# Performance work log

Measured on AMD Instinct MI355X. Metric: run time of the kernel, lower is better.

Reference implementation:

```python
import jax, jax.numpy as jnp
from jax import lax
import numpy as np

NODE_COUNT = 4096
BATCH = 128
THRESHOLD = 1.0
DISSIPATION = 0.1
SPARSITY = 0.9
MAX_ITERS = 100


def setup_inputs() -> dict:
    key = jax.random.key(0)
    k_in, k_conn, k_mask, k_w, k_b = jax.random.split(key, 5)
    input_data = jax.random.normal(k_in, (BATCH, NODE_COUNT), dtype=jnp.float32)
    conn = jax.random.normal(k_conn, (NODE_COUNT, NODE_COUNT), dtype=jnp.float32)
    mask = (jax.random.uniform(k_mask, (NODE_COUNT, NODE_COUNT)) > SPARSITY).astype(jnp.float32)
    conn = conn * mask
    conn = conn / (jnp.abs(conn).sum(axis=1, keepdims=True) + 1e-6)
    # input_proj: Linear(node_count, node_count), torch default init scale
    bound = 1.0 / np.sqrt(NODE_COUNT)
    W = jax.random.uniform(k_w, (NODE_COUNT, NODE_COUNT), minval=-bound, maxval=bound, dtype=jnp.float32)
    b = jax.random.uniform(k_b, (NODE_COUNT,), minval=-bound, maxval=bound, dtype=jnp.float32)
    return {"input_data": input_data, "W": W, "b": b, "connections": conn}


def _avalanche(state, connections):
    """Batched avalanche scan with per-sample sticky early-exit (torch break)."""
    B = state.shape[0]
    done0 = jnp.zeros((B,), dtype=bool)
    total0 = jnp.zeros((B,), dtype=state.dtype)

    def step(carry, _):
        state, done, total = carry
        active = (state > THRESHOLD).astype(state.dtype)          # [B, N]
        n_active = active.sum(axis=1)                              # [B]
        new_done = done | (n_active == 0)                          # break condition
        total = total + jnp.where(new_done, 0.0, n_active)
        # propagated = connections @ active  (per sample)
        prop = jnp.einsum('ij,bj->bi', connections, active)        # [B, N]
        new_state = (state * (1.0 - DISSIPATION) + prop * (1.0 - active)) * (1.0 - active)
        state = jnp.where(new_done[:, None], state, new_state)
        return (state, new_done, total), None

    (state, done, total), _ = lax.scan(step, (state, done0, total0), None, length=MAX_ITERS)
    return state, total


def reference(input_data, W, b, connections):
    projected = input_data @ W.T + b                               # [B, N]
    output, sizes = _avalanche(projected, connections)
    max_size = sizes.max()
    return output, max_size
```

## Files before the change

### kernel.cpp

```cpp
#include <hip/hip_runtime.h>

#define N_NODES 4096
#define BATCH 128
#define SPLITK 16
#define GBN 64
#define GBK 32
#define KCHUNK (N_NODES / SPLITK)
#define NSTEP (KCHUNK / GBK)
#define GEMM_BLOCKS ((N_NODES / GBN) * SPLITK)
#define TRANS_BLOCKS (32 * 32)

typedef _Float16 f16x4 __attribute__((ext_vector_type(4)));
typedef _Float16 f16x8 __attribute__((ext_vector_type(8)));
typedef float f32x4 __attribute__((ext_vector_type(4)));
typedef unsigned int u32x4 __attribute__((ext_vector_type(4)));

__device__ __forceinline__ void dma16(const void* g, void* l) {
#if defined(__has_builtin) && __has_builtin(__builtin_amdgcn_global_load_lds)
  __builtin_amdgcn_global_load_lds((const __attribute__((address_space(1))) void*)g,
                                   (__attribute__((address_space(3))) void*)l, 16, 0, 0);
#else
  *(u32x4*)l = *(const u32x4*)g;
#endif
}

#if defined(__has_builtin)
#if __has_builtin(__builtin_amdgcn_cvt_f32_fp8) && __has_builtin(__builtin_amdgcn_cvt_pk_fp8_f32)
#define CONN_FP8 1
#endif
#endif
#ifndef CONN_FP8
#define CONN_FP8 0
#endif

#if CONN_FP8
#define CONN_ELEM_BYTES 1
#define CONN_SCALE (1.0f / 256.0f)
#else
#define CONN_ELEM_BYTES 2
#define CONN_SCALE 1.0f
#endif

__device__ __forceinline__ void conn_store4(void* out, size_t off, float4 v) {
#if CONN_FP8
  unsigned int p = __builtin_amdgcn_cvt_pk_fp8_f32(v.x * 256.0f, v.y * 256.0f, 0, false);
  p = (unsigned int)__builtin_amdgcn_cvt_pk_fp8_f32(v.z * 256.0f, v.w * 256.0f, (int)p, true);
  *(unsigned int*)((unsigned char*)out + off) = p;
#else
  const unsigned int ux = __float_as_uint(v.x), uy = __float_as_uint(v.y);
  const unsigned int uz = __float_as_uint(v.z), uw = __float_as_uint(v.w);
  ushort4 u;
  u.x = (unsigned short)((ux + 0x7FFFu + ((ux >> 16) & 1u)) >> 16);
  u.y = (unsigned short)((uy + 0x7FFFu + ((uy >> 16) & 1u)) >> 16);
  u.z = (unsigned short)((uz + 0x7FFFu + ((uz >> 16) & 1u)) >> 16);
  u.w = (unsigned short)((uw + 0x7FFFu + ((uw >> 16) & 1u)) >> 16);
  *(ushort4*)((unsigned short*)out + off) = u;
#endif
}

__device__ __forceinline__ float4 conn_load4(const void* cT, int j, int t) {
#if CONN_FP8
  const unsigned int c = *(const unsigned int*)((const unsigned char*)cT + ((size_t)j << 12) + t * 4);
  return make_float4(__builtin_amdgcn_cvt_f32_fp8(c, 0), __builtin_amdgcn_cvt_f32_fp8(c, 1),
                     __builtin_amdgcn_cvt_f32_fp8(c, 2), __builtin_amdgcn_cvt_f32_fp8(c, 3));
#else
  const ushort4 c = *(const ushort4*)((const unsigned short*)cT + ((size_t)j << 12) + t * 4);
  return make_float4(__uint_as_float((unsigned int)c.x << 16),
                     __uint_as_float((unsigned int)c.y << 16),
                     __uint_as_float((unsigned int)c.z << 16),
                     __uint_as_float((unsigned int)c.w << 16));
#endif
}

__global__ __launch_bounds__(256) void asplit_kernel(const float* __restrict__ in,
                                                     _Float16* __restrict__ As,
                                                     unsigned int* __restrict__ maxslot) {
  if (blockIdx.x == 0 && threadIdx.x == 0) *maxslot = 0u;
  const size_t idx = ((size_t)blockIdx.x * 256 + threadIdx.x) * 4;
  const int m = (int)(idx >> 12);
  const int k = (int)(idx & (N_NODES - 1));
  const float4 v = *(const float4*)(in + idx);
  f16x4 hi, lo;
  const float x0 = v.x * 256.f, x1 = v.y * 256.f, x2 = v.z * 256.f, x3 = v.w * 256.f;
  hi[0] = (_Float16)x0; lo[0] = (_Float16)(x0 - (float)hi[0]);
  hi[1] = (_Float16)x1; lo[1] = (_Float16)(x1 - (float)hi[1]);
  hi[2] = (_Float16)x2; lo[2] = (_Float16)(x2 - (float)hi[2]);
  hi[3] = (_Float16)x3; lo[3] = (_Float16)(x3 - (float)hi[3]);
  const size_t base = (size_t)m * 8192 + (size_t)(k >> 5) * 64 + (k & 31);
  *(f16x4*)(As + base) = hi;
  *(f16x4*)(As + base + 32) = lo;
}

__global__ __launch_bounds__(256, 2) void transpose_kernel(const float* __restrict__ conn,
                                                           void* __restrict__ connT) {
  __shared__ float T[128][129];
  const int tid = threadIdx.x;
  const int d = blockIdx.x;
  const int by = (d & 7) | ((d >> 8) << 3);
  const int bx = (d >> 3) & 31;

  const int rr = tid >> 4;
  const int c0 = (tid & 15) * 4;
#pragma unroll
  for (int pass = 0; pass < 8; ++pass) {
    const int r = pass * 16 + rr;
    const float* src = conn + (size_t)(by * 128 + r) * N_NODES + bx * 128;
    const float4 a = *(const float4*)(src + c0);
    const float4 b = *(const float4*)(src + c0 + 64);
    *(float4*)&T[r][c0] = a;
    *(float4*)&T[r][c0 + 64] = b;
  }
  __syncthreads();

  const int jr = tid >> 5;
  const int lc = tid & 31;
#pragma unroll
  for (int pass = 0; pass < 16; ++pass) {
    const int jj = pass * 8 + jr;
    float4 v;
    v.x = T[lc * 4 + 0][jj];
    v.y = T[lc * 4 + 1][jj];
    v.z = T[lc * 4 + 2][jj];
    v.w = T[lc * 4 + 3][jj];
    conn_store4(connT, (size_t)(bx * 128 + jj) * N_NODES + by * 128 + lc * 4, v);
  }
}

struct GemmSmem {
  alignas(16) _Float16 A[128 * 64];
  alignas(16) float B[GBN * 32];
};

__global__ __launch_bounds__(256, 4) void gemm_kernel(const _Float16* __restrict__ As,
                                                      const float* __restrict__ W,
                                                      float* __restrict__ P) {
  __shared__ GemmSmem sm;
  const int tid = threadIdx.x;
  const int bid = blockIdx.x;
  const int kidx = bid & 15;
  const int ntile = bid >> 4;
  const int wave = tid >> 6, lane = tid & 63;
  const int wm = wave >> 1, wn = wave & 1;
  const int g = lane >> 4, lrow = lane & 15;
  const int n0 = ntile * GBN;
  const int kb = kidx * KCHUNK;
  const int crow = lane >> 3;
  const int q = lane & 7;

  auto issue = [&](int t) {
    const size_t abyte = (size_t)((kb >> 5) + t) * 128;
    const size_t bbyte = (size_t)(kb + t * GBK) * 4;
#pragma unroll
    for (int i = 0; i < 4; ++i) {
      const int c = wave * 4 + i;
      const int row = c * 8 + crow;
      dma16((const char*)As + (size_t)row * 16384 + abyte + ((q ^ crow) << 4),
            (char*)sm.A + c * 1024 + lane * 16);
    }
#pragma unroll
    for (int i = 0; i < 2; ++i) {
      const int c = wave * 2 + i;
      const int row = c * 8 + crow;
      dma16((const char*)W + (size_t)(n0 + row) * 16384 + bbyte + ((q ^ crow) << 4),
            (char*)sm.B + c * 1024 + lane * 16);
    }
  };

  f32x4 acc[4][2] = {};

#pragma unroll
  for (int t = 0; t < NSTEP; ++t) {
    issue(t);
    __syncthreads();

    f16x8 ah[4], al[4];
#pragma unroll
    for (int fm = 0; fm < 4; ++fm) {
      const int mr = wm * 64 + fm * 16 + lrow;
      const char* ab = (const char*)sm.A + mr * 128;
      const int s = (mr & 7) << 4;
      ah[fm] = *(const f16x8*)(ab + ((g << 4) ^ s));
      al[fm] = *(const f16x8*)(ab + (((4 + g) << 4) ^ s));
    }
    f16x8 bh[2], bl[2];
#pragma unroll
    for (int fn = 0; fn < 2; ++fn) {
      const int nr = wn * 32 + fn * 16 + lrow;
      const char* bb = (const char*)sm.B + nr * 128;
      const int s = (nr & 7) << 4;
      const f32x4 b0 = *(const f32x4*)(bb + (((2 * g) << 4) ^ s));
      const f32x4 b1 = *(const f32x4*)(bb + (((2 * g + 1) << 4) ^ s));
#pragma unroll
      for (int j = 0; j < 4; ++j) {
        const float x = b0[j] * 64.f;
        const _Float16 h = (_Float16)x;
        bh[fn][j] = h; bl[fn][j] = (_Float16)(x - (float)h);
        const float y = b1[j] * 64.f;
        const _Float16 h2 = (_Float16)y;
        bh[fn][4 + j] = h2; bl[fn][4 + j] = (_Float16)(y - (float)h2);
      }
    }
#pragma unroll
    for (int fm = 0; fm < 4; ++fm)
#pragma unroll
      for (int fn = 0; fn < 2; ++fn) {
        acc[fm][fn] = __builtin_amdgcn_mfma_f32_16x16x32_f16(ah[fm], bh[fn], acc[fm][fn], 0, 0, 0);
        acc[fm][fn] = __builtin_amdgcn_mfma_f32_16x16x32_f16(ah[fm], bl[fn], acc[fm][fn], 0, 0, 0);
        acc[fm][fn] = __builtin_amdgcn_mfma_f32_16x16x32_f16(al[fm], bh[fn], acc[fm][fn], 0, 0, 0);
      }
    __syncthreads();
  }

  constexpr float INV = 1.0f / 16384.0f;
  float* Pb = P + (size_t)kidx * BATCH * N_NODES;
#pragma unroll
  for (int fm = 0; fm < 4; ++fm)
#pragma unroll
    for (int fn = 0; fn < 2; ++fn) {
      const int n = n0 + wn * 32 + fn * 16 + lrow;
#pragma unroll
      for (int reg = 0; reg < 4; ++reg) {
        const int m = wm * 64 + fm * 16 + g * 4 + reg;
        Pb[(size_t)m * N_NODES + n] = acc[fm][fn][reg] * INV;
      }
    }
}

__global__ __launch_bounds__(256) void proj_gemm_valu(const float* __restrict__ A,
                                                      const float* __restrict__ W,
                                                      float* __restrict__ P,
                                                      unsigned int* __restrict__ maxslot) {
  if (blockIdx.x == 0 && threadIdx.x == 0) *maxslot = 0u;
  __shared__ float Asb[16][132];
  __shared__ float Bsb[16][68];
  const int tid = threadIdx.x;
  const int n0 = blockIdx.x * 64;
  const int tx = tid & 15, ty = tid >> 4;
  const int arow = tid >> 1, acol = (tid & 1) * 8;
  const int brow = tid >> 2, bcol = (tid & 3) * 4;
  float acc[2][4][4] = {};
  const float* Aptr = A + (size_t)arow * N_NODES + acol;
  const float* Wptr = W + (size_t)(n0 + brow) * N_NODES + bcol;
  for (int k0 = 0; k0 < N_NODES; k0 += 16) {
    const float4 a0 = *(const float4*)(Aptr + k0);
    const float4 a1 = *(const float4*)(Aptr + k0 + 4);
    const float4 bv = *(const float4*)(Wptr + k0);
    __syncthreads();
    Asb[acol + 0][arow] = a0.x; Asb[acol + 1][arow] = a0.y;
    Asb[acol + 2][arow] = a0.z; Asb[acol + 3][arow] = a0.w;
    Asb[acol + 4][arow] = a1.x; Asb[acol + 5][arow] = a1.y;
    Asb[acol + 6][arow] = a1.z; Asb[acol + 7][arow] = a1.w;
    Bsb[bcol + 0][brow] = bv.x; Bsb[bcol + 1][brow] = bv.y;
    Bsb[bcol + 2][brow] = bv.z; Bsb[bcol + 3][brow] = bv.w;
    __syncthreads();
#pragma unroll
    for (int kk = 0; kk < 16; ++kk) {
      const float4 av0 = *(const float4*)&Asb[kk][ty * 4];
      const float4 av1 = *(const float4*)&Asb[kk][64 + ty * 4];
      const float4 bv4 = *(const float4*)&Bsb[kk][tx * 4];
      const float am[8] = {av0.x, av0.y, av0.z, av0.w, av1.x, av1.y, av1.z, av1.w};
      const float bn[4] = {bv4.x, bv4.y, bv4.z, bv4.w};
#pragma unroll
      for (int i2 = 0; i2 < 2; ++i2)
#pragma unroll
        for (int i = 0; i < 4; ++i)
#pragma unroll
          for (int j = 0; j < 4; ++j)
            acc[i2][i][j] += am[i2 * 4 + i] * bn[j];
    }
  }
#pragma unroll
  for (int i2 = 0; i2 < 2; ++i2)
#pragma unroll
    for (int i = 0; i < 4; ++i) {
      const int m = i2 * 64 + ty * 4 + i;
      *(float4*)(P + (size_t)m * N_NODES + n0 + tx * 4) =
          make_float4(acc[i2][i][0], acc[i2][i][1], acc[i2][i][2], acc[i2][i][3]);
    }
}

__global__ __launch_bounds__(256) void bias_inplace_kernel(float* __restrict__ P,
                                                           const float* __restrict__ bias) {
  const size_t base = ((size_t)blockIdx.x * 256 + threadIdx.x) * 4;
  const int n = (int)(base & (N_NODES - 1));
  float4 s = *(const float4*)(P + base);
  const float4 bv = *(const float4*)(bias + n);
  s.x += bv.x; s.y += bv.y; s.z += bv.z; s.w += bv.w;
  *(float4*)(P + base) = s;
}

template <int MODE, int NSPLIT>
__global__ __launch_bounds__(1024) void avalanche_kernel(const float* __restrict__ Pin,
                                                         const float* __restrict__ bias,
                                                         const void* __restrict__ connv,
                                                         float* __restrict__ out,
                                                         unsigned int* __restrict__ maxslot) {
  const int b = blockIdx.x;
  const int t = threadIdx.x;
  __shared__ unsigned long long mask[64];
  __shared__ int wincl[64];
  __shared__ int list[N_NODES];

  float4 s;
  if (MODE == 1) {
    const float4 bv = *(const float4*)(bias + t * 4);
    s = bv;
#pragma unroll
    for (int sp = 0; sp < NSPLIT; ++sp) {
      const float4 v = *(const float4*)(Pin + (size_t)sp * BATCH * N_NODES +
                                        (size_t)b * N_NODES + t * 4);
      s.x += v.x; s.y += v.y; s.z += v.z; s.w += v.w;
    }
  } else {
    s = *(const float4*)(Pin + (size_t)b * N_NODES + t * 4);
  }

  float total = 0.0f;

  for (int it = 0; it < 100; ++it) {
    const float v0 = s.x, v1 = s.y, v2 = s.z, v3 = s.w;
    unsigned int bits = 0;
    if (v0 > 1.0f) bits |= 1u;
    if (v1 > 1.0f) bits |= 2u;
    if (v2 > 1.0f) bits |= 4u;
    if (v3 > 1.0f) bits |= 8u;

    __syncthreads();
    if (t < 64) mask[t] = 0ULL;
    __syncthreads();
    if (bits) atomicOr(&mask[t >> 4], (unsigned long long)bits << ((t & 15) * 4));
    __syncthreads();

    if (t < 64) {
      int incl = __popcll(mask[t]);
#pragma unroll
      for (int d = 1; d < 64; d <<= 1) {
        const int y = __shfl_up(incl, d);
        if (t >= d) incl += y;
      }
      wincl[t] = incl;
    }
    __syncthreads();
    const int n = wincl[63];
    if (n == 0) break;
    total += (float)n;

    if (t < 64) {
      unsigned long long m = mask[t];
      int o = wincl[t] - __popcll(m);
      while (m) {
        list[o++] = (t << 6) + __builtin_ctzll(m);
        m &= m - 1;
      }
    }
    __syncthreads();

    float4 a0 = make_float4(0.f, 0.f, 0.f, 0.f), a1 = a0, a2 = a0, a3 = a0;
    if (MODE == 1) {
      int idx = 0;
      for (; idx + 8 <= n; idx += 8) {
        const float4 c0 = conn_load4(connv, list[idx + 0], t);
        const float4 c1 = conn_load4(connv, list[idx + 1], t);
        const float4 c2 = conn_load4(connv, list[idx + 2], t);
        const float4 c3 = conn_load4(connv, list[idx + 3], t);
        const float4 c4 = conn_load4(connv, list[idx + 4], t);
        const float4 c5 = conn_load4(connv, list[idx + 5], t);
        const float4 c6 = conn_load4(connv, list[idx + 6], t);
        const float4 c7 = conn_load4(connv, list[idx + 7], t);
        a0.x += c0.x; a0.y += c0.y; a0.z += c0.z; a0.w += c0.w;
        a1.x += c1.x; a1.y += c1.y; a1.z += c1.z; a1.w += c1.w;
        a2.x += c2.x; a2.y += c2.y; a2.z += c2.z; a2.w += c2.w;
        a3.x += c3.x; a3.y += c3.y; a3.z += c3.z; a3.w += c3.w;
        a0.x += c4.x; a0.y += c4.y; a0.z += c4.z; a0.w += c4.w;
        a1.x += c5.x; a1.y += c5.y; a1.z += c5.z; a1.w += c5.w;
        a2.x += c6.x; a2.y += c6.y; a2.z += c6.z; a2.w += c6.w;
        a3.x += c7.x; a3.y += c7.y; a3.z += c7.z; a3.w += c7.w;
      }
      for (; idx < n; ++idx) {
        const float4 c = conn_load4(connv, list[idx], t);
        a0.x += c.x; a0.y += c.y; a0.z += c.z; a0.w += c.w;
      }
    } else {
      const float* conn = (const float*)connv;
      for (int idx = 0; idx < n; ++idx) {
        const int j = list[idx];
        a0.x += conn[(size_t)(t * 4 + 0) * N_NODES + j];
        a0.y += conn[(size_t)(t * 4 + 1) * N_NODES + j];
        a0.z += conn[(size_t)(t * 4 + 2) * N_NODES + j];
        a0.w += conn[(size_t)(t * 4 + 3) * N_NODES + j];
      }
    }
    const float sc = (MODE == 1) ? CONN_SCALE : 1.0f;
    const float4 acc = make_float4(((a0.x + a1.x) + (a2.x + a3.x)) * sc,
                                   ((a0.y + a1.y) + (a2.y + a3.y)) * sc,
                                   ((a0.z + a1.z) + (a2.z + a3.z)) * sc,
                                   ((a0.w + a1.w) + (a2.w + a3.w)) * sc);

    s.x = (v0 > 1.0f) ? 0.0f : 0.9f * v0 + acc.x;
    s.y = (v1 > 1.0f) ? 0.0f : 0.9f * v1 + acc.y;
    s.z = (v2 > 1.0f) ? 0.0f : 0.9f * v2 + acc.z;
    s.w = (v3 > 1.0f) ? 0.0f : 0.9f * v3 + acc.w;
  }

  *(float4*)(out + (size_t)b * N_NODES + t * 4) = s;
  if (t == 0) atomicMax(maxslot, __float_as_uint(total));
}

extern "C" void kernel_launch(void* const* d_in, const int* in_sizes, int n_in,
                              void* d_out, int out_size, void* d_ws, size_t ws_size,
                              hipStream_t stream) {
  const float* input = (const float*)d_in[0];
  const float* W     = (const float*)d_in[1];
  const float* bias  = (const float*)d_in[2];
  const float* conn  = (const float*)d_in[3];
  float* out = (float*)d_out;

  const size_t aplane_bytes = (size_t)BATCH * N_NODES * 4;
  const size_t connT_bytes  = (size_t)N_NODES * N_NODES * CONN_ELEM_BYTES;
  const size_t part_bytes   = (size_t)SPLITK * BATCH * N_NODES * sizeof(float);
  unsigned int* maxslot = (unsigned int*)(out + (size_t)BATCH * N_NODES);

  if (ws_size >= aplane_bytes + connT_bytes + part_bytes) {
    _Float16* As = (_Float16*)d_ws;
    void* connT  = (char*)d_ws + aplane_bytes;
    float* part  = (float*)((char*)d_ws + aplane_bytes + connT_bytes);
    asplit_kernel<<<BATCH * N_NODES / 1024, 256, 0, stream>>>(input, As, maxslot);
    transpose_kernel<<<TRANS_BLOCKS, 256, 0, stream>>>(conn, connT);
    gemm_kernel<<<GEMM_BLOCKS, 256, 0, stream>>>(As, W, part);
    avalanche_kernel<1, SPLITK><<<BATCH, 1024, 0, stream>>>(part, bias, connT, out, maxslot);
  } else {
    proj_gemm_valu<<<dim3(N_NODES / 64, 1), 256, 0, stream>>>(input, W, out, maxslot);
    bias_inplace_kernel<<<BATCH * N_NODES / 1024, 256, 0, stream>>>(out, bias);
    avalanche_kernel<0, 1><<<BATCH, 1024, 0, stream>>>(out, nullptr, conn, out, maxslot);
  }
}
```

Before: 71.19 us.

## Restructure projection GEMM: stage whole A k-chunk in LDS, stream W from registers

Each 512-thread block now loads its full 128x256 fp16 A k-chunk into LDS once (128 KB), then each wave reads its W rows directly from global into registers and runs all 8 k-steps without per-step barriers. The old version double-staged both A and W tiles through LDS with a sync per 32-wide k-step across 1024 smaller blocks. This removes the per-step synchronisation and the W staging. In exchange it uses 256 blocks with one block per CU, large LDS use and high register pressure (acc[8][2]), so latency hiding may suffer.

```diff
diff --git a/kernel.cpp b/kernel.cpp
--- a/kernel.cpp
+++ b/kernel.cpp
@@ -3,11 +3,8 @@
 #define N_NODES 4096
 #define BATCH 128
 #define SPLITK 16
-#define GBN 64
-#define GBK 32
 #define KCHUNK (N_NODES / SPLITK)
-#define NSTEP (KCHUNK / GBK)
-#define GEMM_BLOCKS ((N_NODES / GBN) * SPLITK)
+#define GEMM_BLOCKS 256
 #define TRANS_BLOCKS (32 * 32)
 
 typedef _Float16 f16x4 __attribute__((ext_vector_type(4)));
@@ -126,101 +123,78 @@
   }
 }
 
-struct GemmSmem {
-  alignas(16) _Float16 A[128 * 64];
-  alignas(16) float B[GBN * 32];
-};
-
-__global__ __launch_bounds__(256, 4) void gemm_kernel(const _Float16* __restrict__ As,
+__global__ __launch_bounds__(512, 1) void gemm_kernel(const _Float16* __restrict__ As,
                                                       const float* __restrict__ W,
                                                       float* __restrict__ P) {
-  __shared__ GemmSmem sm;
+  __shared__ _Float16 smA[128 * 512];
   const int tid = threadIdx.x;
   const int bid = blockIdx.x;
   const int kidx = bid & 15;
-  const int ntile = bid >> 4;
+  const int G = bid >> 4;
   const int wave = tid >> 6, lane = tid & 63;
-  const int wm = wave >> 1, wn = wave & 1;
   const int g = lane >> 4, lrow = lane & 15;
-  const int n0 = ntile * GBN;
   const int kb = kidx * KCHUNK;
-  const int crow = lane >> 3;
-  const int q = lane & 7;
-
-  auto issue = [&](int t) {
-    const size_t abyte = (size_t)((kb >> 5) + t) * 128;
-    const size_t bbyte = (size_t)(kb + t * GBK) * 4;
-#pragma unroll
-    for (int i = 0; i < 4; ++i) {
-      const int c = wave * 4 + i;
-      const int row = c * 8 + crow;
-      dma16((const char*)As + (size_t)row * 16384 + abyte + ((q ^ crow) << 4),
-            (char*)sm.A + c * 1024 + lane * 16);
-    }
-#pragma unroll
-    for (int i = 0; i < 2; ++i) {
-      const int c = wave * 2 + i;
-      const int row = c * 8 + crow;
-      dma16((const char*)W + (size_t)(n0 + row) * 16384 + bbyte + ((q ^ crow) << 4),
-            (char*)sm.B + c * 1024 + lane * 16);
-    }
-  };
-
-  f32x4 acc[4][2] = {};
-
-#pragma unroll
-  for (int t = 0; t < NSTEP; ++t) {
-    issue(t);
-    __syncthreads();
-
-    f16x8 ah[4], al[4];
-#pragma unroll
-    for (int fm = 0; fm < 4; ++fm) {
-      const int mr = wm * 64 + fm * 16 + lrow;
-      const char* ab = (const char*)sm.A + mr * 128;
-      const int s = (mr & 7) << 4;
-      ah[fm] = *(const f16x8*)(ab + ((g << 4) ^ s));
-      al[fm] = *(const f16x8*)(ab + (((4 + g) << 4) ^ s));
-    }
+
+#pragma unroll
+  for (int p = 0; p < 16; ++p) {
+    const int off = p * 8192 + tid * 16;
+    const int m = off >> 10;
+    const int g64 = (off >> 4) & 63;
+    const int kg = g64 >> 3, q = g64 & 7;
+    dma16((const char*)As + (size_t)m * 16384 + (size_t)(kidx * 8 + kg) * 128 +
+              ((q ^ (m & 7)) << 4),
+          (char*)smA + off);
+  }
+  __syncthreads();
+
+  const int n0w = G * 256 + wave * 32;
+  const float* Wl0 = W + (size_t)(n0w + lrow) * N_NODES + kb + g * 8;
+  const float* Wl1 = W + (size_t)(n0w + 16 + lrow) * N_NODES + kb + g * 8;
+
+  f32x4 acc[8][2] = {};
+
+#pragma unroll
+  for (int kk = 0; kk < 8; ++kk) {
+    const f32x4 b00 = *(const f32x4*)(Wl0 + kk * 32);
+    const f32x4 b01 = *(const f32x4*)(Wl0 + kk * 32 + 4);
+    const f32x4 b10 = *(const f32x4*)(Wl1 + kk * 32);
+    const f32x4 b11 = *(const f32x4*)(Wl1 + kk * 32 + 4);
     f16x8 bh[2], bl[2];
 #pragma unroll
-    for (int fn = 0; fn < 2; ++fn) {
-      const int nr = wn * 32 + fn * 16 + lrow;
-      const char* bb = (const char*)sm.B + nr * 128;
-      const int s = (nr & 7) << 4;
-      const f32x4 b0 = *(const f32x4*)(bb + (((2 * g) << 4) ^ s));
-      const f32x4 b1 = *(const f32x4*)(bb + (((2 * g + 1) << 4) ^ s));
-#pragma unroll
-      for (int j = 0; j < 4; ++j) {
-        const float x = b0[j] * 64.f;
-        const _Float16 h = (_Float16)x;
-        bh[fn][j] = h; bl[fn][j] = (_Float16)(x - (float)h);
-        const float y = b1[j] * 64.f;
-        const _Float16 h2 = (_Float16)y;
-        bh[fn][4 + j] = h2; bl[fn][4 + j] = (_Float16)(y - (float)h2);
-      }
-    }
-#pragma unroll
-    for (int fm = 0; fm < 4; ++fm)
+    for (int j = 0; j < 4; ++j) {
+      float x;
+      _Float16 h;
+      x = b00[j] * 64.f; h = (_Float16)x; bh[0][j] = h; bl[0][j] = (_Float16)(x - (float)h);
+      x = b01[j] * 64.f; h = (_Float16)x; bh[0][4 + j] = h; bl[0][4 + j] = (_Float16)(x - (float)h);
+      x = b10[j] * 64.f; h = (_Float16)x; bh[1][j] = h; bl[1][j] = (_Float16)(x - (float)h);
+      x = b11[j] * 64.f; h = (_Float16)x; bh[1][4 + j] = h; bl[1][4 + j] = (_Float16)(x - (float)h);
+    }
+#pragma unroll
+    for (int fm = 0; fm < 8; ++fm) {
+      const int m = fm * 16 + lrow;
+      const char* ab = (const char*)smA + m * 1024 + kk * 128;
+      const int s = m & 7;
+      const f16x8 ah = *(const f16x8*)(ab + ((g ^ s) << 4));
+      const f16x8 al = *(const f16x8*)(ab + (((4 + g) ^ s) << 4));
 #pragma unroll
       for (int fn = 0; fn < 2; ++fn) {
-        acc[fm][fn] = __builtin_amdgcn_mfma_f32_16x16x32_f16(ah[fm], bh[fn], acc[fm][fn], 0, 0, 0);
-        acc[fm][fn] = __builtin_amdgcn_mfma_f32_16x16x32_f16(ah[fm], bl[fn], acc[fm][fn], 0, 0, 0);
-        acc[fm][fn] = __builtin_amdgcn_mfma_f32_16x16x32_f16(al[fm], bh[fn], acc[fm][fn], 0, 0, 0);
-      }
-    __syncthreads();
+        acc[fm][fn] = __builtin_amdgcn_mfma_f32_16x16x32_f16(ah, bh[fn], acc[fm][fn], 0, 0, 0);
+        acc[fm][fn] = __builtin_amdgcn_mfma_f32_16x16x32_f16(ah, bl[fn], acc[fm][fn], 0, 0, 0);
+        acc[fm][fn] = __builtin_amdgcn_mfma_f32_16x16x32_f16(al, bh[fn], acc[fm][fn], 0, 0, 0);
+      }
+    }
   }
 
   constexpr float INV = 1.0f / 16384.0f;
   float* Pb = P + (size_t)kidx * BATCH * N_NODES;
 #pragma unroll
-  for (int fm = 0; fm < 4; ++fm)
+  for (int fm = 0; fm < 8; ++fm)
 #pragma unroll
     for (int fn = 0; fn < 2; ++fn) {
-      const int n = n0 + wn * 32 + fn * 16 + lrow;
+      const int n = n0w + fn * 16 + lrow;
 #pragma unroll
       for (int reg = 0; reg < 4; ++reg) {
-        const int m = wm * 64 + fm * 16 + g * 4 + reg;
+        const int m = fm * 16 + g * 4 + reg;
         Pb[(size_t)m * N_NODES + n] = acc[fm][fn][reg] * INV;
       }
     }
@@ -426,7 +400,7 @@
     float* part  = (float*)((char*)d_ws + aplane_bytes + connT_bytes);
     asplit_kernel<<<BATCH * N_NODES / 1024, 256, 0, stream>>>(input, As, maxslot);
     transpose_kernel<<<TRANS_BLOCKS, 256, 0, stream>>>(conn, connT);
-    gemm_kernel<<<GEMM_BLOCKS, 256, 0, stream>>>(As, W, part);
+    gemm_kernel<<<GEMM_BLOCKS, 512, 0, stream>>>(As, W, part);
     avalanche_kernel<1, SPLITK><<<BATCH, 1024, 0, stream>>>(part, bias, connT, out, maxslot);
   } else {
     proj_gemm_valu<<<dim3(N_NODES / 64, 1), 256, 0, stream>>>(input, W, out, maxslot);
```

New measurement: 69.98 us. Within noise of the previous version (-1.7%).
